# Kernel tuning notes

Hardware: AMD Instinct MI355X
Metric: run time of the kernel (lower is better)

## Reference

```python
import math
import jax, jax.numpy as jnp
import numpy as np

H = 32          # query heads
KV = 8          # key/value heads (GQA)
D = 128         # head_dim
PAGE = 16       # Quest page size
TOPK = 256      # page budget
THETA = 10000.0


def _rope(x, pos):
    # x: [..., D]; llama rotate_half RoPE at scalar position pos
    half = D // 2
    inv = 1.0 / (THETA ** (jnp.arange(half, dtype=jnp.float32) * 2.0 / D))
    ang = pos * inv                                   # [half]
    cos = jnp.concatenate([jnp.cos(ang), jnp.cos(ang)])  # [D]
    sin = jnp.concatenate([jnp.sin(ang), jnp.sin(ang)])
    rot = jnp.concatenate([-x[..., half:], x[..., :half]], axis=-1)
    return x * cos + rot * sin


def setup_inputs() -> dict:
    key = jax.random.key(0)
    ks = jax.random.split(key, 7)
    hid = H * D
    s = 1.0 / math.sqrt(hid)
    return {
        "hidden_states": jax.random.normal(ks[0], (1, 1, hid), jnp.float32),
        "k_cache": jax.random.normal(ks[1], (32767, KV, D), jnp.float32),
        "v_cache": jax.random.normal(ks[2], (32767, KV, D), jnp.float32),
        "Wq": jax.random.normal(ks[3], (hid, H * D), jnp.float32) * s,
        "Wk": jax.random.normal(ks[4], (hid, KV * D), jnp.float32) * s,
        "Wv": jax.random.normal(ks[5], (hid, KV * D), jnp.float32) * s,
        "Wo": jax.random.normal(ks[6], (H * D, hid), jnp.float32) * s,
    }


def reference(hidden_states, k_cache, v_cache, Wq, Wk, Wv, Wo):
    x = hidden_states[0]                    # [1, hidden]
    q = (x @ Wq).reshape(H, D)              # decode: q_len == 1
    k = (x @ Wk).reshape(KV, D)
    v = (x @ Wv).reshape(KV, D)

    past = k_cache.shape[0]
    q = _rope(q, jnp.float32(past))
    k = _rope(k, jnp.float32(past))

    # append_kv: paged cache, seqlen = past + 1 = n_pages * PAGE
    Kc = jnp.concatenate([k_cache, k[None]], axis=0)   # [S, KV, D]
    Vc = jnp.concatenate([v_cache, v[None]], axis=0)
    S = past + 1
    n_pages = S // PAGE

    # decode_estimate: per-page min/max key metadata, Quest upper-bound score
    Kp = Kc.reshape(n_pages, PAGE, KV, D)
    kmax = Kp.max(axis=1)                   # [P, KV, D]
    kmin = Kp.min(axis=1)
    G = H // KV
    qh = q.reshape(KV, G, D)
    pmax = qh[None] * kmax[:, :, None, :]   # [P, KV, G, D]
    pmin = qh[None] * kmin[:, :, None, :]
    score = jnp.maximum(pmax, pmin).sum(-1) # [P, KV, G]
    score = score.reshape(n_pages, H).T     # [H, P]
    # most recent page always attended
    score = score.at[:, -1].set(jnp.inf)

    # decode_topk: per-head page selection
    _, pidx = jax.lax.top_k(score, TOPK)    # [H, TOPK]
    tok = (pidx[..., None] * PAGE + jnp.arange(PAGE)).reshape(H, -1)  # [H, T]

    # decode_sparse_attn: gather selected pages (GQA mapping) + attention
    kvmap = jnp.arange(H) // G              # query head -> kv head
    Ksel = Kc[tok, kvmap[:, None]]          # [H, T, D]
    Vsel = Vc[tok, kvmap[:, None]]
    att = jnp.einsum('hd,htd->ht', q, Ksel) * (1.0 / math.sqrt(D))
    w = jax.nn.softmax(att, axis=-1)
    out = jnp.einsum('ht,htd->hd', w, Vsel) # [H, D]

    y = out.reshape(1, H * D) @ Wo          # o_proj
    return y[None]                          # [1, 1, hidden]
```

## Files before the change

kernel.cpp:

```cpp
#include <hip/hip_runtime.h>
#include <math.h>

#define H 32
#define KV 8
#define D 128
#define PAGE 16
#define TOPK 256
#define NPAGES 2048
#define PAST 32767
#define HID 4096

#define WS_Q       0
#define WS_K       4096
#define WS_V       5120
#define WS_SCORES  6144
#define WS_PIDX    71680
#define WS_PART_M  79872
#define WS_PART_L  80896
#define WS_PART_O  81920
#define WS_QKVPART 212992
#define WS_WOPART  606208

#define NCHUNK 32
#define PPC    8

__global__ void qkv1_kernel(const float* __restrict__ x,
                            const float* __restrict__ Wq,
                            const float* __restrict__ Wk,
                            const float* __restrict__ Wv,
                            float* __restrict__ part) {
    __shared__ float xs[64];
    int tid = threadIdx.x;
    int rc = blockIdx.x / 6;
    int cg = blockIdx.x % 6;
    int r0 = rc * 64;
    if (tid < 64) xs[tid] = x[r0 + tid];
    __syncthreads();
    const float* W; int Cc; int col; int gcol;
    if (cg < 4)       { W = Wq; Cc = 4096; col = cg * 1024 + tid * 4; gcol = col; }
    else if (cg == 4) { W = Wk; Cc = 1024; col = tid * 4;             gcol = 4096 + col; }
    else              { W = Wv; Cc = 1024; col = tid * 4;             gcol = 5120 + col; }
    const float* Wp = W + (size_t)r0 * Cc + col;
    float4 acc = {0.f, 0.f, 0.f, 0.f};
#pragma unroll 8
    for (int r = 0; r < 64; ++r) {
        float4 w4 = *(const float4*)(Wp + (size_t)r * Cc);
        float xr = xs[r];
        acc.x = fmaf(xr, w4.x, acc.x);
        acc.y = fmaf(xr, w4.y, acc.y);
        acc.z = fmaf(xr, w4.z, acc.z);
        acc.w = fmaf(xr, w4.w, acc.w);
    }
    *(float4*)(part + (size_t)rc * 6144 + gcol) = acc;
}

__global__ void reduce_rope_kernel(const float* __restrict__ part,
                                   float* __restrict__ qkv) {
    __shared__ float smem[256];
    int tid = threadIdx.x;
    int c = blockIdx.x * 256 + tid;
    float s = 0.f;
#pragma unroll 8
    for (int rc = 0; rc < 64; ++rc) s += part[(size_t)rc * 6144 + c];
    smem[tid] = s;
    __syncthreads();
    float outv;
    if (c < 5120) {
        int j = c & 127;
        int jj = (j < 64) ? j : (j - 64);
        double t = (double)jj / 64.0;
        float p = (float)pow(10000.0, t);
        float invf = 1.0f / p;
        float ang = 32767.0f * invf;
        float co = (float)cos((double)ang);
        float si = (float)sin((double)ang);
        if (j < 64) { float x0 = s, x1 = smem[tid + 64]; outv = x0 * co - x1 * si; }
        else        { float x1 = s, x0 = smem[tid - 64]; outv = x1 * co + x0 * si; }
    } else {
        outv = s;
    }
    qkv[c] = outv;
}

__global__ void score_kernel(const float* __restrict__ kc,
                             const float* __restrict__ q,
                             float* __restrict__ scores) {
    int tid = threadIdx.x;
    int lane = tid & 63;
    int wv = tid >> 6;
    int sub = lane & 31;
    int hf = lane >> 5;
    int p = blockIdx.x >> 1;
    int kv = ((blockIdx.x & 1) << 2) + wv;
    const float* kp0 = kc + ((size_t)(p * PAGE) * KV + kv) * D + 4 * sub;
    float4 mx = {-INFINITY, -INFINITY, -INFINITY, -INFINITY};
    float4 mn = { INFINITY,  INFINITY,  INFINITY,  INFINITY};
#pragma unroll
    for (int s8 = 0; s8 < 8; ++s8) {
        int t = 2 * s8 + hf;
        float4 v = *(const float4*)(kp0 + (size_t)t * (KV * D));
        mx.x = fmaxf(mx.x, v.x); mn.x = fminf(mn.x, v.x);
        mx.y = fmaxf(mx.y, v.y); mn.y = fminf(mn.y, v.y);
        mx.z = fmaxf(mx.z, v.z); mn.z = fminf(mn.z, v.z);
        mx.w = fmaxf(mx.w, v.w); mn.w = fminf(mn.w, v.w);
    }
    mx.x = fmaxf(mx.x, __shfl_xor(mx.x, 32)); mn.x = fminf(mn.x, __shfl_xor(mn.x, 32));
    mx.y = fmaxf(mx.y, __shfl_xor(mx.y, 32)); mn.y = fminf(mn.y, __shfl_xor(mn.y, 32));
    mx.z = fmaxf(mx.z, __shfl_xor(mx.z, 32)); mn.z = fminf(mn.z, __shfl_xor(mn.z, 32));
    mx.w = fmaxf(mx.w, __shfl_xor(mx.w, 32)); mn.w = fminf(mn.w, __shfl_xor(mn.w, 32));
    float sacc[4];
#pragma unroll
    for (int g = 0; g < 4; ++g) {
        float4 qq = *(const float4*)(q + (size_t)(kv * 4 + g) * 128 + 4 * sub);
        sacc[g] = fmaxf(qq.x * mx.x, qq.x * mn.x) + fmaxf(qq.y * mx.y, qq.y * mn.y)
                + fmaxf(qq.z * mx.z, qq.z * mn.z) + fmaxf(qq.w * mx.w, qq.w * mn.w);
    }
#pragma unroll
    for (int off = 16; off > 0; off >>= 1) {
#pragma unroll
        for (int g = 0; g < 4; ++g) sacc[g] += __shfl_xor(sacc[g], off);
    }
    if (lane == 0) {
#pragma unroll
        for (int g = 0; g < 4; ++g)
            scores[(size_t)(kv * 4 + g) * NPAGES + p] = sacc[g];
    }
}

__global__ void topk_kernel(const float* __restrict__ scores, int* __restrict__ pidx) {
    __shared__ unsigned su[NPAGES];
    __shared__ int hist[256];
    __shared__ int scan[256];
    __shared__ int wtot[4];
    __shared__ int cnt;
    __shared__ unsigned s_prefix;
    __shared__ int s_k;
    int tid = threadIdx.x;
    int lane = tid & 63;
    int wv = tid >> 6;
    int h = blockIdx.x;
    for (int i = tid; i < NPAGES; i += 256) {
        unsigned u;
        if (i == NPAGES - 1) u = 0xFFFFFFFFu;
        else {
            int b = __float_as_int(scores[(size_t)h * NPAGES + i]);
            u = (b >= 0) ? ((unsigned)b | 0x80000000u) : ~(unsigned)b;
        }
        su[i] = u;
    }
    if (tid == 0) cnt = 0;
    __syncthreads();

    unsigned prefix = 0;
    int K = TOPK;
    for (int level = 3; level >= 0; --level) {
        int shift = level * 8;
        unsigned pmask = (level == 3) ? 0u : (0xFFFFFFFFu << (shift + 8));
        hist[tid] = 0;
        __syncthreads();
        for (int i = tid; i < NPAGES; i += 256) {
            unsigned u = su[i];
            if ((u & pmask) == prefix)
                atomicAdd(&hist[(u >> shift) & 0xFF], 1);
        }
        __syncthreads();
        int v = hist[tid];
#pragma unroll
        for (int off = 1; off < 64; off <<= 1) {
            int o = __shfl_down(v, off);
            if (lane + off < 64) v += o;
        }
        if (lane == 0) wtot[wv] = v;
        __syncthreads();
        int add = 0;
        for (int w2 = wv + 1; w2 < 4; ++w2) add += wtot[w2];
        v += add;
        scan[tid] = v;
        __syncthreads();
        int nxt = (tid < 255) ? scan[tid + 1] : 0;
        if (v >= K && nxt < K) {
            s_prefix = prefix | ((unsigned)tid << shift);
            s_k = K - nxt;
        }
        __syncthreads();
        prefix = s_prefix;
        K = s_k;
        __syncthreads();
    }
    unsigned T = prefix;

    for (int i = tid; i < NPAGES; i += 256) {
        if (su[i] > T) {
            int pos = atomicAdd(&cnt, 1);
            pidx[h * TOPK + pos] = i;
        }
    }
    int base = TOPK - K;
    int i0 = tid * (NPAGES / 256);
    int tcount = 0;
#pragma unroll
    for (int j = 0; j < NPAGES / 256; ++j) if (su[i0 + j] == T) ++tcount;
    int sc = tcount;
#pragma unroll
    for (int off = 1; off < 64; off <<= 1) {
        int o = __shfl_up(sc, off);
        if (lane >= off) sc += o;
    }
    __syncthreads();
    if (lane == 63) wtot[wv] = sc;
    __syncthreads();
    int wadd = 0;
    for (int w2 = 0; w2 < wv; ++w2) wadd += wtot[w2];
    int pos = base + (sc - tcount) + wadd;
#pragma unroll
    for (int j = 0; j < NPAGES / 256; ++j) {
        if (su[i0 + j] == T) {
            if (pos < TOPK) pidx[h * TOPK + pos] = i0 + j;
            ++pos;
        }
    }
}

__global__ void attn_kernel(const float* __restrict__ kc,
                            const float* __restrict__ vc,
                            const float* __restrict__ ws,
                            const int* __restrict__ pidx,
                            float* __restrict__ part_m,
                            float* __restrict__ part_l,
                            float* __restrict__ part_o) {
    int tid = threadIdx.x;
    int lane = tid & 63;
    int wv = tid >> 6;
    int sub = lane & 31;
    int hf = lane >> 5;
    int h = blockIdx.x >> 5;
    int c = blockIdx.x & 31;
    int kvh = h >> 2;
    __shared__ float qs[128];
    __shared__ float sm[8], sl[8];
    __shared__ float so[8 * 128];
    if (tid < 128) qs[tid] = ws[WS_Q + h * 128 + tid];
    __syncthreads();
    float4 q4 = *(const float4*)(qs + 4 * sub);
    int hidx = wv * 2 + hf;
    int page = pidx[h * TOPK + c * PPC + hidx];
    size_t base = ((size_t)(page * PAGE) * KV + kvh) * D + 4 * sub;
    bool last = (page == NPAGES - 1);
    const float scale = 0.08838834764831843f;

    float s[PAGE];
#pragma unroll
    for (int t = 0; t < PAGE; ++t) {
        const float* kp = (last && t == PAGE - 1) ? (ws + WS_K + kvh * 128 + 4 * sub)
                                                  : (kc + base + (size_t)t * (KV * D));
        float4 kk = *(const float4*)kp;
        float d = q4.x * kk.x + q4.y * kk.y + q4.z * kk.z + q4.w * kk.w;
#pragma unroll
        for (int off = 16; off > 0; off >>= 1) d += __shfl_xor(d, off);
        s[t] = d * scale;
    }
    float m = -INFINITY;
#pragma unroll
    for (int t = 0; t < PAGE; ++t) m = fmaxf(m, s[t]);
    float l = 0.f;
    float4 o = {0.f, 0.f, 0.f, 0.f};
#pragma unroll
    for (int t = 0; t < PAGE; ++t) {
        float w = __expf(s[t] - m);
        l += w;
        const float* vp = (last && t == PAGE - 1) ? (ws + WS_V + kvh * 128 + 4 * sub)
                                                  : (vc + base + (size_t)t * (KV * D));
        float4 vv = *(const float4*)vp;
        o.x = fmaf(w, vv.x, o.x);
        o.y = fmaf(w, vv.y, o.y);
        o.z = fmaf(w, vv.z, o.z);
        o.w = fmaf(w, vv.w, o.w);
    }
    if (sub == 0) { sm[hidx] = m; sl[hidx] = l; }
    *(float4*)(so + hidx * 128 + 4 * sub) = o;
    __syncthreads();
    if (tid < 128) {
        float M = -INFINITY;
#pragma unroll
        for (int w2 = 0; w2 < 8; ++w2) M = fmaxf(M, sm[w2]);
        float L = 0.f, O = 0.f;
#pragma unroll
        for (int w2 = 0; w2 < 8; ++w2) {
            float f = __expf(sm[w2] - M);
            L += f * sl[w2];
            O += f * so[w2 * 128 + tid];
        }
        int pc = h * NCHUNK + c;
        if (tid == 0) { part_m[pc] = M; part_l[pc] = L; }
        part_o[(size_t)pc * 128 + tid] = O;
    }
}

__global__ void wo1_kernel(const float* __restrict__ part_m,
                           const float* __restrict__ part_l,
                           const float* __restrict__ part_o,
                           const float* __restrict__ Wo,
                           float* __restrict__ wpart) {
    __shared__ float xs[64];
    int tid = threadIdx.x;
    int rc = blockIdx.x >> 2;
    int cb = blockIdx.x & 3;
    int r0 = rc * 64;
    int h0 = r0 >> 7;
    int dbase = r0 & 127;
    if (tid < 64) {
        int d = dbase + tid;
        float M = -INFINITY;
#pragma unroll
        for (int c = 0; c < NCHUNK; ++c) M = fmaxf(M, part_m[h0 * NCHUNK + c]);
        float L = 0.f, O = 0.f;
#pragma unroll
        for (int c = 0; c < NCHUNK; ++c) {
            float f = __expf(part_m[h0 * NCHUNK + c] - M);
            L += f * part_l[h0 * NCHUNK + c];
            O += f * part_o[(size_t)(h0 * NCHUNK + c) * 128 + d];
        }
        xs[tid] = O / L;
    }
    __syncthreads();
    int col = cb * 1024 + tid * 4;
    const float* Wp = Wo + (size_t)r0 * 4096 + col;
    float4 acc = {0.f, 0.f, 0.f, 0.f};
#pragma unroll 8
    for (int r = 0; r < 64; ++r) {
        float4 w4 = *(const float4*)(Wp + (size_t)r * 4096);
        float xr = xs[r];
        acc.x = fmaf(xr, w4.x, acc.x);
        acc.y = fmaf(xr, w4.y, acc.y);
        acc.z = fmaf(xr, w4.z, acc.z);
        acc.w = fmaf(xr, w4.w, acc.w);
    }
    *(float4*)(wpart + (size_t)rc * 4096 + col) = acc;
}

__global__ void wo2_kernel(const float* __restrict__ wpart,
                           float* __restrict__ out) {
    int tid = threadIdx.x;
    int col = blockIdx.x * 1024 + tid * 4;
    float4 acc = {0.f, 0.f, 0.f, 0.f};
#pragma unroll 8
    for (int rc = 0; rc < 64; ++rc) {
        float4 p = *(const float4*)(wpart + (size_t)rc * 4096 + col);
        acc.x += p.x; acc.y += p.y; acc.z += p.z; acc.w += p.w;
    }
    *(float4*)(out + col) = acc;
}

extern "C" void kernel_launch(void* const* d_in, const int* in_sizes, int n_in,
                              void* d_out, int out_size, void* d_ws, size_t ws_size,
                              hipStream_t stream) {
    const float* x  = (const float*)d_in[0];
    const float* kc = (const float*)d_in[1];
    const float* vc = (const float*)d_in[2];
    const float* Wq = (const float*)d_in[3];
    const float* Wk = (const float*)d_in[4];
    const float* Wv = (const float*)d_in[5];
    const float* Wo = (const float*)d_in[6];
    float* ws = (float*)d_ws;
    float* out = (float*)d_out;

    qkv1_kernel<<<384, 256, 0, stream>>>(x, Wq, Wk, Wv, ws + WS_QKVPART);
    reduce_rope_kernel<<<24, 256, 0, stream>>>(ws + WS_QKVPART, ws + WS_Q);
    score_kernel<<<(NPAGES - 1) * 2, 256, 0, stream>>>(kc, ws + WS_Q, ws + WS_SCORES);
    topk_kernel<<<H, 256, 0, stream>>>(ws + WS_SCORES, (int*)(ws + WS_PIDX));
    attn_kernel<<<H * NCHUNK, 256, 0, stream>>>(kc, vc, ws, (const int*)(ws + WS_PIDX),
                                                ws + WS_PART_M, ws + WS_PART_L, ws + WS_PART_O);
    wo1_kernel<<<256, 256, 0, stream>>>(ws + WS_PART_M, ws + WS_PART_L, ws + WS_PART_O,
                                        Wo, ws + WS_WOPART);
    wo2_kernel<<<4, 256, 0, stream>>>(ws + WS_WOPART, out);
}
```

Measured before the change: 401.3 us.

## Fuse QKV projection with page min/max metadata and precompute RoPE tables

The QKV projection blocks, the per-page key min/max reduction and a RoPE cos/sin table are merged into one launch. The min/max pass no longer waits for q, so it can overlap with the weight GEMV. The score kernel then reads the precomputed kmax/kmin buffers instead of the raw key cache, and the QKV and Wo split-K factors are halved per block to expose more parallelism. In exchange, about 16 MB of kmax/kmin is written to workspace and read back, and the reduce kernels sum over twice as many partials.

```diff
diff --git a/kernel.cpp b/kernel.cpp
--- a/kernel.cpp
+++ b/kernel.cpp
@@ -13,67 +13,98 @@
 #define WS_Q       0
 #define WS_K       4096
 #define WS_V       5120
-#define WS_SCORES  6144
-#define WS_PIDX    71680
-#define WS_PART_M  79872
-#define WS_PART_L  80896
-#define WS_PART_O  81920
-#define WS_QKVPART 212992
-#define WS_WOPART  606208
+#define WS_ROPE    6144
+#define WS_SCORES  6272
+#define WS_PIDX    71808
+#define WS_PART_M  80000
+#define WS_PART_L  81024
+#define WS_PART_O  82048
+#define WS_KMAX    213120
+#define WS_KMIN    2310272
+#define WS_QKVPART 4407424
+#define WS_WOPART  5193856
 
 #define NCHUNK 32
 #define PPC    8
 
-__global__ void qkv1_kernel(const float* __restrict__ x,
-                            const float* __restrict__ Wq,
-                            const float* __restrict__ Wk,
-                            const float* __restrict__ Wv,
-                            float* __restrict__ part) {
-    __shared__ float xs[64];
-    int tid = threadIdx.x;
-    int rc = blockIdx.x / 6;
-    int cg = blockIdx.x % 6;
-    int r0 = rc * 64;
-    if (tid < 64) xs[tid] = x[r0 + tid];
-    __syncthreads();
-    const float* W; int Cc; int col; int gcol;
-    if (cg < 4)       { W = Wq; Cc = 4096; col = cg * 1024 + tid * 4; gcol = col; }
-    else if (cg == 4) { W = Wk; Cc = 1024; col = tid * 4;             gcol = 4096 + col; }
-    else              { W = Wv; Cc = 1024; col = tid * 4;             gcol = 5120 + col; }
-    const float* Wp = W + (size_t)r0 * Cc + col;
-    float4 acc = {0.f, 0.f, 0.f, 0.f};
-#pragma unroll 8
-    for (int r = 0; r < 64; ++r) {
-        float4 w4 = *(const float4*)(Wp + (size_t)r * Cc);
-        float xr = xs[r];
-        acc.x = fmaf(xr, w4.x, acc.x);
-        acc.y = fmaf(xr, w4.y, acc.y);
-        acc.z = fmaf(xr, w4.z, acc.z);
-        acc.w = fmaf(xr, w4.w, acc.w);
-    }
-    *(float4*)(part + (size_t)rc * 6144 + gcol) = acc;
+__global__ void fused1_kernel(const float* __restrict__ x,
+                              const float* __restrict__ Wq,
+                              const float* __restrict__ Wk,
+                              const float* __restrict__ Wv,
+                              const float* __restrict__ kc,
+                              float* __restrict__ ws) {
+    __shared__ float xs[32];
+    int tid = threadIdx.x;
+    int b = blockIdx.x;
+    if (b < 768) {
+        int rc = b / 6;
+        int cg = b % 6;
+        int r0 = rc * 32;
+        if (tid < 32) xs[tid] = x[r0 + tid];
+        __syncthreads();
+        const float* W; int Cc; int col; int gcol;
+        if (cg < 4)       { W = Wq; Cc = 4096; col = cg * 1024 + tid * 4; gcol = col; }
+        else if (cg == 4) { W = Wk; Cc = 1024; col = tid * 4;             gcol = 4096 + col; }
+        else              { W = Wv; Cc = 1024; col = tid * 4;             gcol = 5120 + col; }
+        const float* Wp = W + (size_t)r0 * Cc + col;
+        float4 acc = {0.f, 0.f, 0.f, 0.f};
+#pragma unroll 8
+        for (int r = 0; r < 32; ++r) {
+            float4 w4 = *(const float4*)(Wp + (size_t)r * Cc);
+            float xr = xs[r];
+            acc.x = fmaf(xr, w4.x, acc.x);
+            acc.y = fmaf(xr, w4.y, acc.y);
+            acc.z = fmaf(xr, w4.z, acc.z);
+            acc.w = fmaf(xr, w4.w, acc.w);
+        }
+        *(float4*)(ws + WS_QKVPART + (size_t)rc * 6144 + gcol) = acc;
+    } else if (b < 768 + (NPAGES - 1)) {
+        int p = b - 768;
+        int kv = tid >> 5;
+        int sub = tid & 31;
+        const float* kp = kc + ((size_t)(p * PAGE) * KV + kv) * D + 4 * sub;
+        float4 mx = {-INFINITY, -INFINITY, -INFINITY, -INFINITY};
+        float4 mn = { INFINITY,  INFINITY,  INFINITY,  INFINITY};
+#pragma unroll
+        for (int t = 0; t < PAGE; ++t) {
+            float4 v = *(const float4*)(kp + (size_t)t * (KV * D));
+            mx.x = fmaxf(mx.x, v.x); mn.x = fminf(mn.x, v.x);
+            mx.y = fmaxf(mx.y, v.y); mn.y = fminf(mn.y, v.y);
+            mx.z = fmaxf(mx.z, v.z); mn.z = fminf(mn.z, v.z);
+            mx.w = fmaxf(mx.w, v.w); mn.w = fminf(mn.w, v.w);
+        }
+        size_t o = ((size_t)p * KV + kv) * D + 4 * sub;
+        *(float4*)(ws + WS_KMAX + o) = mx;
+        *(float4*)(ws + WS_KMIN + o) = mn;
+    } else {
+        if (tid < 64) {
+            double t = (double)tid / 64.0;
+            float pw = (float)pow(10000.0, t);
+            float invf = 1.0f / pw;
+            float ang = 32767.0f * invf;
+            ws[WS_ROPE + tid]      = (float)cos((double)ang);
+            ws[WS_ROPE + 64 + tid] = (float)sin((double)ang);
+        }
+    }
 }
 
 __global__ void reduce_rope_kernel(const float* __restrict__ part,
+                                   const float* __restrict__ rope,
                                    float* __restrict__ qkv) {
     __shared__ float smem[256];
     int tid = threadIdx.x;
     int c = blockIdx.x * 256 + tid;
     float s = 0.f;
 #pragma unroll 8
-    for (int rc = 0; rc < 64; ++rc) s += part[(size_t)rc * 6144 + c];
+    for (int rc = 0; rc < 128; ++rc) s += part[(size_t)rc * 6144 + c];
     smem[tid] = s;
     __syncthreads();
     float outv;
     if (c < 5120) {
         int j = c & 127;
-        int jj = (j < 64) ? j : (j - 64);
-        double t = (double)jj / 64.0;
-        float p = (float)pow(10000.0, t);
-        float invf = 1.0f / p;
-        float ang = 32767.0f * invf;
-        float co = (float)cos((double)ang);
-        float si = (float)sin((double)ang);
+        int jj = j & 63;
+        float co = rope[jj];
+        float si = rope[64 + jj];
         if (j < 64) { float x0 = s, x1 = smem[tid + 64]; outv = x0 * co - x1 * si; }
         else        { float x1 = s, x0 = smem[tid - 64]; outv = x1 * co + x0 * si; }
     } else {
@@ -82,49 +113,29 @@
     qkv[c] = outv;
 }
 
-__global__ void score_kernel(const float* __restrict__ kc,
+__global__ void score_kernel(const float* __restrict__ kmaxb,
+                             const float* __restrict__ kminb,
                              const float* __restrict__ q,
                              float* __restrict__ scores) {
     int tid = threadIdx.x;
-    int lane = tid & 63;
-    int wv = tid >> 6;
-    int sub = lane & 31;
-    int hf = lane >> 5;
-    int p = blockIdx.x >> 1;
-    int kv = ((blockIdx.x & 1) << 2) + wv;
-    const float* kp0 = kc + ((size_t)(p * PAGE) * KV + kv) * D + 4 * sub;
-    float4 mx = {-INFINITY, -INFINITY, -INFINITY, -INFINITY};
-    float4 mn = { INFINITY,  INFINITY,  INFINITY,  INFINITY};
-#pragma unroll
-    for (int s8 = 0; s8 < 8; ++s8) {
-        int t = 2 * s8 + hf;
-        float4 v = *(const float4*)(kp0 + (size_t)t * (KV * D));
-        mx.x = fmaxf(mx.x, v.x); mn.x = fminf(mn.x, v.x);
-        mx.y = fmaxf(mx.y, v.y); mn.y = fminf(mn.y, v.y);
-        mx.z = fmaxf(mx.z, v.z); mn.z = fminf(mn.z, v.z);
-        mx.w = fmaxf(mx.w, v.w); mn.w = fminf(mn.w, v.w);
-    }
-    mx.x = fmaxf(mx.x, __shfl_xor(mx.x, 32)); mn.x = fminf(mn.x, __shfl_xor(mn.x, 32));
-    mx.y = fmaxf(mx.y, __shfl_xor(mx.y, 32)); mn.y = fminf(mn.y, __shfl_xor(mn.y, 32));
-    mx.z = fmaxf(mx.z, __shfl_xor(mx.z, 32)); mn.z = fminf(mn.z, __shfl_xor(mn.z, 32));
-    mx.w = fmaxf(mx.w, __shfl_xor(mx.w, 32)); mn.w = fminf(mn.w, __shfl_xor(mn.w, 32));
-    float sacc[4];
-#pragma unroll
-    for (int g = 0; g < 4; ++g) {
-        float4 qq = *(const float4*)(q + (size_t)(kv * 4 + g) * 128 + 4 * sub);
-        sacc[g] = fmaxf(qq.x * mx.x, qq.x * mn.x) + fmaxf(qq.y * mx.y, qq.y * mn.y)
-                + fmaxf(qq.z * mx.z, qq.z * mn.z) + fmaxf(qq.w * mx.w, qq.w * mn.w);
-    }
-#pragma unroll
-    for (int off = 16; off > 0; off >>= 1) {
-#pragma unroll
-        for (int g = 0; g < 4; ++g) sacc[g] += __shfl_xor(sacc[g], off);
-    }
-    if (lane == 0) {
-#pragma unroll
-        for (int g = 0; g < 4; ++g)
-            scores[(size_t)(kv * 4 + g) * NPAGES + p] = sacc[g];
-    }
+    int pl = tid & 7;
+    int h  = tid >> 3;
+    int kv = h >> 2;
+    int p  = blockIdx.x * 8 + pl;
+    if (p >= NPAGES - 1) return;
+    const float* qp  = q + (size_t)h * D;
+    const float* kmx = kmaxb + ((size_t)p * KV + kv) * D;
+    const float* kmn = kminb + ((size_t)p * KV + kv) * D;
+    float acc = 0.f;
+#pragma unroll 8
+    for (int d0 = 0; d0 < 32; ++d0) {
+        float4 qq = *(const float4*)(qp + 4 * d0);
+        float4 a  = *(const float4*)(kmx + 4 * d0);
+        float4 bb = *(const float4*)(kmn + 4 * d0);
+        acc += fmaxf(qq.x * a.x, qq.x * bb.x) + fmaxf(qq.y * a.y, qq.y * bb.y)
+             + fmaxf(qq.z * a.z, qq.z * bb.z) + fmaxf(qq.w * a.w, qq.w * bb.w);
+    }
+    scores[(size_t)h * NPAGES + p] = acc;
 }
 
 __global__ void topk_kernel(const float* __restrict__ scores, int* __restrict__ pidx) {
@@ -301,14 +312,14 @@
                            const float* __restrict__ part_o,
                            const float* __restrict__ Wo,
                            float* __restrict__ wpart) {
-    __shared__ float xs[64];
+    __shared__ float xs[32];
     int tid = threadIdx.x;
     int rc = blockIdx.x >> 2;
     int cb = blockIdx.x & 3;
-    int r0 = rc * 64;
+    int r0 = rc * 32;
     int h0 = r0 >> 7;
     int dbase = r0 & 127;
-    if (tid < 64) {
+    if (tid < 32) {
         int d = dbase + tid;
         float M = -INFINITY;
 #pragma unroll
@@ -327,7 +338,7 @@
     const float* Wp = Wo + (size_t)r0 * 4096 + col;
     float4 acc = {0.f, 0.f, 0.f, 0.f};
 #pragma unroll 8
-    for (int r = 0; r < 64; ++r) {
+    for (int r = 0; r < 32; ++r) {
         float4 w4 = *(const float4*)(Wp + (size_t)r * 4096);
         float xr = xs[r];
         acc.x = fmaf(xr, w4.x, acc.x);
@@ -341,14 +352,11 @@
 __global__ void wo2_kernel(const float* __restrict__ wpart,
                            float* __restrict__ out) {
     int tid = threadIdx.x;
-    int col = blockIdx.x * 1024 + tid * 4;
-    float4 acc = {0.f, 0.f, 0.f, 0.f};
-#pragma unroll 8
-    for (int rc = 0; rc < 64; ++rc) {
-        float4 p = *(const float4*)(wpart + (size_t)rc * 4096 + col);
-        acc.x += p.x; acc.y += p.y; acc.z += p.z; acc.w += p.w;
-    }
-    *(float4*)(out + col) = acc;
+    int col = blockIdx.x * 256 + tid;
+    float acc = 0.f;
+#pragma unroll 8
+    for (int rc = 0; rc < 128; ++rc) acc += wpart[(size_t)rc * 4096 + col];
+    out[col] = acc;
 }
 
 extern "C" void kernel_launch(void* const* d_in, const int* in_sizes, int n_in,
@@ -364,13 +372,13 @@
     float* ws = (float*)d_ws;
     float* out = (float*)d_out;
 
-    qkv1_kernel<<<384, 256, 0, stream>>>(x, Wq, Wk, Wv, ws + WS_QKVPART);
-    reduce_rope_kernel<<<24, 256, 0, stream>>>(ws + WS_QKVPART, ws + WS_Q);
-    score_kernel<<<(NPAGES - 1) * 2, 256, 0, stream>>>(kc, ws + WS_Q, ws + WS_SCORES);
+    fused1_kernel<<<768 + (NPAGES - 1) + 1, 256, 0, stream>>>(x, Wq, Wk, Wv, kc, ws);
+    reduce_rope_kernel<<<24, 256, 0, stream>>>(ws + WS_QKVPART, ws + WS_ROPE, ws + WS_Q);
+    score_kernel<<<256, 256, 0, stream>>>(ws + WS_KMAX, ws + WS_KMIN, ws + WS_Q, ws + WS_SCORES);
     topk_kernel<<<H, 256, 0, stream>>>(ws + WS_SCORES, (int*)(ws + WS_PIDX));
     attn_kernel<<<H * NCHUNK, 256, 0, stream>>>(kc, vc, ws, (const int*)(ws + WS_PIDX),
                                                 ws + WS_PART_M, ws + WS_PART_L, ws + WS_PART_O);
-    wo1_kernel<<<256, 256, 0, stream>>>(ws + WS_PART_M, ws + WS_PART_L, ws + WS_PART_O,
+    wo1_kernel<<<512, 256, 0, stream>>>(ws + WS_PART_M, ws + WS_PART_L, ws + WS_PART_O,
                                         Wo, ws + WS_WOPART);
-    wo2_kernel<<<4, 256, 0, stream>>>(ws + WS_WOPART, out);
-}
+    wo2_kernel<<<16, 256, 0, stream>>>(ws + WS_WOPART, out);
+}
```

New measurement: 417.5 us. 4.0% more time.
